# Optimization experiments

Measured on AMD Instinct MI355X. Metric: run time of the kernel, lower is better.

Reference implementation:

```python
import jax, jax.numpy as jnp
import numpy as np

N, F_IN, F_OUT, K = 4096, 32, 32, 2
NEG_SLOPE = 0.2
MASK_VAL = -9e15


def _sparse_mat(kv, km, density=0.01):
    vals = jax.random.normal(kv, (N, N), dtype=jnp.float32)
    mask = jax.random.uniform(km, (N, N)) < density
    return vals * mask


def setup_inputs() -> dict:
    key = jax.random.key(0)
    ks = jax.random.split(key, 12)
    x = jax.random.normal(ks[0], (N, F_IN), dtype=jnp.float32)
    Ld = _sparse_mat(ks[1], ks[2])
    Lu = _sparse_mat(ks[3], ks[4])
    P = jax.random.normal(ks[5], (N, N), dtype=jnp.float32) / np.sqrt(N)
    W1 = jax.random.normal(ks[6], (K, F_IN, F_OUT), dtype=jnp.float32) * 0.1
    W2 = jax.random.normal(ks[7], (K, F_IN, F_OUT), dtype=jnp.float32) * 0.1
    W0 = jax.random.normal(ks[8], (F_IN, F_OUT), dtype=jnp.float32) * 0.1
    att1 = jax.random.normal(ks[9], (2 * F_OUT * K, 1), dtype=jnp.float32) * 0.1
    att2 = jax.random.normal(ks[10], (2 * F_OUT * K, 1), dtype=jnp.float32) * 0.1
    return {"x": x, "Ld": Ld, "Lu": Lu, "P": P, "W1": W1, "W2": W2,
            "W0": W0, "att1": att1, "att2": att2}


def _branch(x, L, W, att):
    # W: [K, F_in, F_out]; precompute x @ W[k] for all k -> [K, N, F_out]
    Kk, _, Fo = W.shape
    xw = jnp.einsum('nf,kfo->kno', x, W)
    # torch.cat([x@W[k]], dim=1) == transpose+reshape of xw
    xcat = jnp.transpose(xw, (1, 0, 2)).reshape(x.shape[0], Kk * Fo)
    d = Fo * Kk
    e = xcat @ att[:d] + (xcat @ att[d:]).T            # [N, N]
    e = jax.nn.leaky_relu(e, negative_slope=NEG_SLOPE)
    e = jnp.where(L != 0, e, MASK_VAL)
    alpha = jax.nn.softmax(e, axis=1)                   # row softmax, no dropout (eval)
    z = alpha @ xw[0]
    a = alpha
    for k in range(1, Kk):
        a = a @ L
        z = z + a @ xw[k]
    return z


def reference(x, Ld, Lu, P, W1, W2, W0, att1, att2):
    z1 = _branch(x, Ld, W1, att1)
    z2 = _branch(x, Lu, W2, att2)
    x0 = P @ (x @ W0)
    return z1 + z2 + x0
```

## Files before the change

kernel.cpp:

```cpp
#include <hip/hip_runtime.h>
#include <hip/hip_bf16.h>

#define NN 4096
#define CAP 128
#define KS 8

typedef __attribute__((ext_vector_type(8))) short bf16x8;
typedef __attribute__((ext_vector_type(4))) float f32x4;

__device__ __forceinline__ float lrelu(float v) { return v >= 0.f ? v : 0.2f * v; }

__device__ __forceinline__ ushort f2bu(float f) {
    unsigned u = __float_as_uint(f);
    return (ushort)((u + 0x7FFFu + ((u >> 16) & 1u)) >> 16);
}

__global__ __launch_bounds__(256) void k_prep(
    const float* __restrict__ x,
    const float* __restrict__ W1, const float* __restrict__ W2,
    const float* __restrict__ W0,
    const float* __restrict__ att1, const float* __restrict__ att2,
    float* __restrict__ xwA1, float* __restrict__ xwB1,
    float* __restrict__ xwA2, float* __restrict__ xwB2,
    float* __restrict__ a1, float* __restrict__ b1,
    float* __restrict__ a2, float* __restrict__ b2,
    __hip_bfloat16* __restrict__ Bt)
{
    __shared__ float wl[5120];
    __shared__ float xs[256];
    const int t = threadIdx.x;
    for (int i = t; i < 2048; i += 256) { wl[i] = W1[i]; wl[2048 + i] = W2[i]; }
    for (int i = t; i < 1024; i += 256) wl[4096 + i] = W0[i];
    const int rowBase = blockIdx.x * 8;
    xs[t] = x[rowBase * 32 + t];
    __syncthreads();

    const int o = t & 31, r = t >> 5;
    const int row = rowBase + r;
    const float* xr = &xs[r * 32];
    float vA1 = 0.f, vB1 = 0.f, vA2 = 0.f, vB2 = 0.f, v0 = 0.f;
#pragma unroll
    for (int f = 0; f < 32; ++f) {
        const float xv = xr[f];
        vA1 += xv * wl[f * 32 + o];
        vB1 += xv * wl[1024 + f * 32 + o];
        vA2 += xv * wl[2048 + f * 32 + o];
        vB2 += xv * wl[3072 + f * 32 + o];
        v0  += xv * wl[4096 + f * 32 + o];
    }
    xwA1[row * 32 + o] = vA1;
    xwB1[row * 32 + o] = vB1;
    xwA2[row * 32 + o] = vA2;
    xwB2[row * 32 + o] = vB2;
    ((ushort*)Bt)[(size_t)o * NN + row] = f2bu(v0);

    float pa1 = vA1 * att1[o]      + vB1 * att1[32 + o];
    float pb1 = vA1 * att1[64 + o] + vB1 * att1[96 + o];
    float pa2 = vA2 * att2[o]      + vB2 * att2[32 + o];
    float pb2 = vA2 * att2[64 + o] + vB2 * att2[96 + o];
#pragma unroll
    for (int m = 1; m <= 16; m <<= 1) {
        pa1 += __shfl_xor(pa1, m); pb1 += __shfl_xor(pb1, m);
        pa2 += __shfl_xor(pa2, m); pb2 += __shfl_xor(pb2, m);
    }
    if (o == 0) { a1[row] = pa1; b1[row] = pb1; a2[row] = pa2; b2[row] = pb2; }
}

__global__ __launch_bounds__(256) void k_scan(
    const float* __restrict__ Ld, const float* __restrict__ Lu,
    const float* __restrict__ xwB1, const float* __restrict__ xwB2,
    int* __restrict__ csr, int* __restrict__ cntArr,
    float* __restrict__ y1, float* __restrict__ y2)
{
    const int row = blockIdx.x;
    const int br  = blockIdx.y;
    const float* L   = br ? Lu : Ld;
    const float* xwB = br ? xwB2 : xwB1;
    int*   csrB = csr + (size_t)br * NN * CAP;
    int*   cntB = cntArr + br * NN;
    float* y    = br ? y2 : y1;

    __shared__ int   sidx[CAP];
    __shared__ float sval[CAP];
    __shared__ int   scnt;
    __shared__ float red[256];
    const int t = threadIdx.x;
    const int lane = t & 63;
    if (t == 0) scnt = 0;
    __syncthreads();

    const float4* L4 = (const float4*)(L + (size_t)row * NN);
    float4 v[4];
#pragma unroll
    for (int it = 0; it < 4; ++it) v[it] = L4[it * 256 + t];

    const unsigned long long lt = (1ull << lane) - 1ull;
#pragma unroll
    for (int it = 0; it < 4; ++it) {
        const float vx = v[it].x, vy = v[it].y, vz = v[it].z, vw = v[it].w;
        const unsigned long long m0 = __ballot(vx != 0.f);
        const unsigned long long m1 = __ballot(vy != 0.f);
        const unsigned long long m2 = __ballot(vz != 0.f);
        const unsigned long long m3 = __ballot(vw != 0.f);
        const int p0 = __popcll(m0), p1 = __popcll(m1), p2 = __popcll(m2);
        const int tot = p0 + p1 + p2 + __popcll(m3);
        int base = 0;
        if (lane == 0 && tot) base = atomicAdd(&scnt, tot);
        base = __shfl(base, 0);
        const int c0 = (it * 256 + t) * 4;
        int s;
        s = base + __popcll(m0 & lt);
        if (vx != 0.f && s < CAP) { sidx[s] = c0;     sval[s] = vx; }
        s = base + p0 + __popcll(m1 & lt);
        if (vy != 0.f && s < CAP) { sidx[s] = c0 + 1; sval[s] = vy; }
        s = base + p0 + p1 + __popcll(m2 & lt);
        if (vz != 0.f && s < CAP) { sidx[s] = c0 + 2; sval[s] = vz; }
        s = base + p0 + p1 + p2 + __popcll(m3 & lt);
        if (vw != 0.f && s < CAP) { sidx[s] = c0 + 3; sval[s] = vw; }
    }
    __syncthreads();
    const int cnt = min(scnt, CAP);
    for (int s = t; s < cnt; s += 256) csrB[(size_t)row * CAP + s] = sidx[s];
    if (t == 0) cntB[row] = cnt;

    const int o = t & 31, g = t >> 5;
    float acc = 0.f;
    for (int s = g; s < cnt; s += 8) acc += sval[s] * xwB[(size_t)sidx[s] * 32 + o];
    red[t] = acc;
    __syncthreads();
    if (t < 32) {
        float tot2 = 0.f;
#pragma unroll
        for (int g2 = 0; g2 < 8; ++g2) tot2 += red[g2 * 32 + t];
        y[(size_t)row * 32 + t] = tot2;
    }
}

__global__ __launch_bounds__(256) void k_attn(
    const int* __restrict__ csr, const int* __restrict__ cntArr,
    const float* __restrict__ a1, const float* __restrict__ b1,
    const float* __restrict__ a2, const float* __restrict__ b2,
    const float* __restrict__ xwA1, const float* __restrict__ xwA2,
    const float* __restrict__ y1, const float* __restrict__ y2,
    float* __restrict__ z1, float* __restrict__ z2)
{
    const int br = blockIdx.y;
    const int* csrB = csr + (size_t)br * NN * CAP;
    const int* cntB = cntArr + br * NN;
    const float* aA  = br ? a2 : a1;
    const float* bA  = br ? b2 : b1;
    const float* xwA = br ? xwA2 : xwA1;
    const float* y   = br ? y2 : y1;
    float* z = br ? z2 : z1;

    __shared__ float elds[4 * CAP];
    const int w = threadIdx.x >> 6, lane = threadIdx.x & 63;
    const int row = blockIdx.x * 4 + w;
    const int cnt = cntB[row];
    const float ai = aA[row];
    const int* ci = csrB + (size_t)row * CAP;
    float* ew = elds + w * CAP;

    float lmax = -1e30f;
    for (int s = lane; s < cnt; s += 64) {
        const float e = lrelu(ai + bA[ci[s]]);
        ew[s] = e;
        lmax = fmaxf(lmax, e);
    }
#pragma unroll
    for (int m = 1; m <= 32; m <<= 1) lmax = fmaxf(lmax, __shfl_xor(lmax, m));
    float ssum = 0.f;
    for (int s = lane; s < cnt; s += 64) ssum += __expf(ew[s] - lmax);
#pragma unroll
    for (int m = 1; m <= 32; m <<= 1) ssum += __shfl_xor(ssum, m);

    const int h = lane >> 5, o = lane & 31;
    float acc = 0.f;
    for (int s = h; s < cnt; s += 2) {
        const float wgt = __expf(ew[s] - lmax);
        const int col = ci[s];
        acc += wgt * (xwA[(size_t)col * 32 + o] + y[(size_t)col * 32 + o]);
    }
    acc += __shfl_xor(acc, 32);
    if (lane < 32) z[(size_t)row * 32 + o] = (cnt > 0) ? acc / ssum : 0.f;
}

__global__ __launch_bounds__(256) void k_pgemm(
    const float* __restrict__ P, const ushort* __restrict__ Bt,
    float* __restrict__ partial)
{
    __shared__ ushort sA[2][16 * 64 * 8];
    __shared__ ushort sB[2][8 * 64 * 8];
    const int t = threadIdx.x;
    const int row0 = blockIdx.x * 64;
    const int ks = blockIdx.y;
    const float4*  P4  = (const float4*)P;
    const ushort4* Bt4 = (const ushort4*)Bt;

    const int lane = t & 63, w = t >> 6;

    f32x4 acc0 = {0.f, 0.f, 0.f, 0.f};
    f32x4 acc1 = {0.f, 0.f, 0.f, 0.f};

    auto stageA = [&](int c, int buf) {
        const int kc4 = (ks * 512 + c * 128) >> 2;
#pragma unroll
        for (int j = 0; j < 8; ++j) {
            const int i = t + 256 * j;
            const int row = i >> 5, q = i & 31;
            const float4 v = P4[(size_t)(row0 + row) * 1024 + kc4 + q];
            ushort4 u;
            u.x = f2bu(v.x); u.y = f2bu(v.y); u.z = f2bu(v.z); u.w = f2bu(v.w);
            const int wi = row >> 4, m = row & 15;
            const int kk = q >> 3, quad = (q >> 1) & 3, jj = q & 1;
            *(ushort4*)&sA[buf][(((wi * 4 + kk) * 64) + quad * 16 + m) * 8 + jj * 4] = u;
        }
    };
    auto stageB = [&](int c, int buf) {
        const int kc4 = (ks * 512 + c * 128) >> 2;
#pragma unroll
        for (int j = 0; j < 4; ++j) {
            const int i = t + 256 * j;
            const int o = i >> 5, q = i & 31;
            const ushort4 u = Bt4[(size_t)o * 1024 + kc4 + q];
            const int nt = o >> 4, n = o & 15;
            const int kk = q >> 3, quad = (q >> 1) & 3, jj = q & 1;
            *(ushort4*)&sB[buf][(((kk * 2 + nt) * 64) + quad * 16 + n) * 8 + jj * 4] = u;
        }
    };
    auto compute = [&](int buf) {
        const ushort* pa = &sA[buf][(w * 4) * 64 * 8 + lane * 8];
        const ushort* pb = &sB[buf][lane * 8];
#pragma unroll
        for (int kk = 0; kk < 4; ++kk) {
            const bf16x8 a  = *(const bf16x8*)(pa + kk * 512);
            const bf16x8 b0 = *(const bf16x8*)(pb + kk * 1024);
            const bf16x8 b1 = *(const bf16x8*)(pb + kk * 1024 + 512);
            acc0 = __builtin_amdgcn_mfma_f32_16x16x32_bf16(a, b0, acc0, 0, 0, 0);
            acc1 = __builtin_amdgcn_mfma_f32_16x16x32_bf16(a, b1, acc1, 0, 0, 0);
        }
    };

    stageA(0, 0); stageB(0, 0);
    __syncthreads();
    for (int c = 0; c < 4; ++c) {
        if (c < 3) { stageA(c + 1, (c + 1) & 1); stageB(c + 1, (c + 1) & 1); }
        compute(c & 1);
        __syncthreads();
    }

    const int m = lane & 15, quad = lane >> 4;
    float* out = partial + ((size_t)ks * NN + row0 + w * 16 + quad * 4) * 32;
#pragma unroll
    for (int r = 0; r < 4; ++r) {
        out[r * 32 + m]      = acc0[r];
        out[r * 32 + 16 + m] = acc1[r];
    }
}

__global__ __launch_bounds__(256) void k_combine(
    const float4* __restrict__ z1, const float4* __restrict__ z2,
    const float4* __restrict__ partial, float4* __restrict__ out)
{
    const int i = blockIdx.x * 256 + threadIdx.x;
    const float4 a = z1[i], b = z2[i];
    float rx = a.x + b.x, ry = a.y + b.y, rz = a.z + b.z, rw = a.w + b.w;
#pragma unroll
    for (int p = 0; p < KS; ++p) {
        const float4 c = partial[p * 32768 + i];
        rx += c.x; ry += c.y; rz += c.z; rw += c.w;
    }
    float4 rr; rr.x = rx; rr.y = ry; rr.z = rz; rr.w = rw;
    out[i] = rr;
}

extern "C" void kernel_launch(void* const* d_in, const int* in_sizes, int n_in,
                              void* d_out, int out_size, void* d_ws, size_t ws_size,
                              hipStream_t stream) {
    (void)in_sizes; (void)n_in; (void)out_size; (void)ws_size;
    const float* x    = (const float*)d_in[0];
    const float* Ld   = (const float*)d_in[1];
    const float* Lu   = (const float*)d_in[2];
    const float* P    = (const float*)d_in[3];
    const float* W1   = (const float*)d_in[4];
    const float* W2   = (const float*)d_in[5];
    const float* W0   = (const float*)d_in[6];
    const float* att1 = (const float*)d_in[7];
    const float* att2 = (const float*)d_in[8];

    float* ws = (float*)d_ws;
    float* xwA1 = ws;
    float* xwB1 = ws + 131072;
    float* xwA2 = ws + 262144;
    float* xwB2 = ws + 393216;
    float* y1   = ws + 524288;
    float* y2   = ws + 655360;
    float* z1   = ws + 786432;
    float* z2   = ws + 917504;
    float* a1   = ws + 1048576;
    float* b1   = ws + 1052672;
    float* a2   = ws + 1056768;
    float* b2   = ws + 1060864;
    float* partial = ws + 1064960;
    __hip_bfloat16* Bt = (__hip_bfloat16*)(ws + 1064960 + KS * 131072);
    int* csr = (int*)(ws + 1064960 + KS * 131072 + 65536);
    int* cnt = (int*)(ws + 1064960 + KS * 131072 + 65536 + 1048576);

    k_prep<<<512, 256, 0, stream>>>(x, W1, W2, W0, att1, att2,
                                    xwA1, xwB1, xwA2, xwB2, a1, b1, a2, b2, Bt);
    k_scan<<<dim3(NN, 2), 256, 0, stream>>>(Ld, Lu, xwB1, xwB2, csr, cnt, y1, y2);
    k_attn<<<dim3(NN / 4, 2), 256, 0, stream>>>(csr, cnt, a1, b1, a2, b2,
                                                xwA1, xwA2, y1, y2, z1, z2);
    k_pgemm<<<dim3(64, KS), 256, 0, stream>>>(P, (const ushort*)Bt, partial);
    k_combine<<<128, 256, 0, stream>>>((const float4*)z1, (const float4*)z2,
                                       (const float4*)partial, (float4*)d_out);
}
```

Before: 235.4 us.

## Make sparse scan deterministic, prefuse xwA into u, pipeline gathers

In k_scan, the LDS atomic slot allocation is replaced by a per-wave count prefix computed after one barrier, so compaction order becomes deterministic. Entries are zero-padded to a multiple of 16, and the gather-multiply loop is software-pipelined. The xwA term is added into the per-row y vector (now u), so k_attn gathers one array instead of two. k_attn also computes the softmax weights in registers with a fixed two-slot layout and prefetches its gathers a step ahead. The cost is redundant ballots in k_scan and extra work on padded zero entries.

```diff
diff --git a/kernel.cpp b/kernel.cpp
--- a/kernel.cpp
+++ b/kernel.cpp
@@ -69,25 +69,25 @@
 __global__ __launch_bounds__(256) void k_scan(
     const float* __restrict__ Ld, const float* __restrict__ Lu,
     const float* __restrict__ xwB1, const float* __restrict__ xwB2,
+    const float* __restrict__ xwA1, const float* __restrict__ xwA2,
     int* __restrict__ csr, int* __restrict__ cntArr,
-    float* __restrict__ y1, float* __restrict__ y2)
+    float* __restrict__ u1, float* __restrict__ u2)
 {
     const int row = blockIdx.x;
     const int br  = blockIdx.y;
     const float* L   = br ? Lu : Ld;
     const float* xwB = br ? xwB2 : xwB1;
+    const float* xwA = br ? xwA2 : xwA1;
     int*   csrB = csr + (size_t)br * NN * CAP;
     int*   cntB = cntArr + br * NN;
-    float* y    = br ? y2 : y1;
+    float* u    = br ? u2 : u1;
 
     __shared__ int   sidx[CAP];
     __shared__ float sval[CAP];
-    __shared__ int   scnt;
+    __shared__ int   wcnt[16];
     __shared__ float red[256];
     const int t = threadIdx.x;
-    const int lane = t & 63;
-    if (t == 0) scnt = 0;
-    __syncthreads();
+    const int lane = t & 63, w = t >> 6;
 
     const float4* L4 = (const float4*)(L + (size_t)row * NN);
     float4 v[4];
@@ -95,6 +95,38 @@
     for (int it = 0; it < 4; ++it) v[it] = L4[it * 256 + t];
 
     const unsigned long long lt = (1ull << lane) - 1ull;
+
+    int tots[4];
+#pragma unroll
+    for (int it = 0; it < 4; ++it) {
+        const unsigned long long m0 = __ballot(v[it].x != 0.f);
+        const unsigned long long m1 = __ballot(v[it].y != 0.f);
+        const unsigned long long m2 = __ballot(v[it].z != 0.f);
+        const unsigned long long m3 = __ballot(v[it].w != 0.f);
+        tots[it] = __popcll(m0) + __popcll(m1) + __popcll(m2) + __popcll(m3);
+    }
+    if (lane == 0) {
+        int4 tv; tv.x = tots[0]; tv.y = tots[1]; tv.z = tots[2]; tv.w = tots[3];
+        *(int4*)&wcnt[w * 4] = tv;
+    }
+    __syncthreads();
+
+    const int4 ca = *(const int4*)&wcnt[0];
+    const int4 cb = *(const int4*)&wcnt[4];
+    const int4 cc = *(const int4*)&wcnt[8];
+    const int4 cd = *(const int4*)&wcnt[12];
+    const int cs[16] = {ca.x, ca.y, ca.z, ca.w, cb.x, cb.y, cb.z, cb.w,
+                        cc.x, cc.y, cc.z, cc.w, cd.x, cd.y, cd.z, cd.w};
+    int total = 0;
+#pragma unroll
+    for (int k2 = 0; k2 < 16; ++k2) total += cs[k2];
+    int base = 0;
+#pragma unroll
+    for (int k2 = 0; k2 < 16; ++k2) base += (k2 < (w << 2)) ? cs[k2] : 0;
+
+    const int cnt  = min(total, CAP);
+    const int cp16 = min((cnt + 15) & ~15, CAP);
+
 #pragma unroll
     for (int it = 0; it < 4; ++it) {
         const float vx = v[it].x, vy = v[it].y, vz = v[it].z, vw = v[it].w;
@@ -103,10 +135,6 @@
         const unsigned long long m2 = __ballot(vz != 0.f);
         const unsigned long long m3 = __ballot(vw != 0.f);
         const int p0 = __popcll(m0), p1 = __popcll(m1), p2 = __popcll(m2);
-        const int tot = p0 + p1 + p2 + __popcll(m3);
-        int base = 0;
-        if (lane == 0 && tot) base = atomicAdd(&scnt, tot);
-        base = __shfl(base, 0);
         const int c0 = (it * 256 + t) * 4;
         int s;
         s = base + __popcll(m0 & lt);
@@ -117,22 +145,40 @@
         if (vz != 0.f && s < CAP) { sidx[s] = c0 + 2; sval[s] = vz; }
         s = base + p0 + p1 + p2 + __popcll(m3 & lt);
         if (vw != 0.f && s < CAP) { sidx[s] = c0 + 3; sval[s] = vw; }
-    }
-    __syncthreads();
-    const int cnt = min(scnt, CAP);
-    for (int s = t; s < cnt; s += 256) csrB[(size_t)row * CAP + s] = sidx[s];
-    if (t == 0) cntB[row] = cnt;
+        base += p0 + p1 + p2 + __popcll(m3);
+    }
+    if (t >= cnt && t < cp16) { sidx[t] = 0; sval[t] = 0.f; }
+    __syncthreads();
+
+    if (t < cp16) csrB[(size_t)row * CAP + t] = sidx[t];
+    if (t == 0)   cntB[row] = cnt;
 
     const int o = t & 31, g = t >> 5;
     float acc = 0.f;
-    for (int s = g; s < cnt; s += 8) acc += sval[s] * xwB[(size_t)sidx[s] * 32 + o];
+    const int nPair = cp16 >> 4;
+    if (nPair > 0) {
+        int   iA0 = sidx[g],      iA1 = sidx[g + 8];
+        float vA0 = sval[g],      vA1 = sval[g + 8];
+        float xA0 = xwB[(size_t)iA0 * 32 + o];
+        float xA1 = xwB[(size_t)iA1 * 32 + o];
+        for (int j = 1; j < nPair; ++j) {
+            const int sB = g + 16 * j;
+            const int   iB0 = sidx[sB],  iB1 = sidx[sB + 8];
+            const float vB0 = sval[sB],  vB1 = sval[sB + 8];
+            const float xB0 = xwB[(size_t)iB0 * 32 + o];
+            const float xB1 = xwB[(size_t)iB1 * 32 + o];
+            acc += vA0 * xA0 + vA1 * xA1;
+            vA0 = vB0; xA0 = xB0; vA1 = vB1; xA1 = xB1;
+        }
+        acc += vA0 * xA0 + vA1 * xA1;
+    }
     red[t] = acc;
     __syncthreads();
     if (t < 32) {
         float tot2 = 0.f;
 #pragma unroll
         for (int g2 = 0; g2 < 8; ++g2) tot2 += red[g2 * 32 + t];
-        y[(size_t)row * 32 + t] = tot2;
+        u[(size_t)row * 32 + t] = tot2 + xwA[(size_t)row * 32 + t];
     }
 }
 
@@ -140,46 +186,69 @@
     const int* __restrict__ csr, const int* __restrict__ cntArr,
     const float* __restrict__ a1, const float* __restrict__ b1,
     const float* __restrict__ a2, const float* __restrict__ b2,
-    const float* __restrict__ xwA1, const float* __restrict__ xwA2,
-    const float* __restrict__ y1, const float* __restrict__ y2,
+    const float* __restrict__ u1, const float* __restrict__ u2,
     float* __restrict__ z1, float* __restrict__ z2)
 {
     const int br = blockIdx.y;
     const int* csrB = csr + (size_t)br * NN * CAP;
     const int* cntB = cntArr + br * NN;
-    const float* aA  = br ? a2 : a1;
-    const float* bA  = br ? b2 : b1;
-    const float* xwA = br ? xwA2 : xwA1;
-    const float* y   = br ? y2 : y1;
+    const float* aA = br ? a2 : a1;
+    const float* bA = br ? b2 : b1;
+    const float* U  = br ? u2 : u1;
     float* z = br ? z2 : z1;
 
-    __shared__ float elds[4 * CAP];
+    __shared__ float sw[4 * CAP];
+    __shared__ int   sci[4 * CAP];
     const int w = threadIdx.x >> 6, lane = threadIdx.x & 63;
     const int row = blockIdx.x * 4 + w;
     const int cnt = cntB[row];
+    const int cp16 = min((cnt + 15) & ~15, CAP);
     const float ai = aA[row];
     const int* ci = csrB + (size_t)row * CAP;
-    float* ew = elds + w * CAP;
-
-    float lmax = -1e30f;
-    for (int s = lane; s < cnt; s += 64) {
-        const float e = lrelu(ai + bA[ci[s]]);
-        ew[s] = e;
-        lmax = fmaxf(lmax, e);
-    }
+    float* swg = sw + w * CAP;
+    int*   scg = sci + w * CAP;
+
+    int id0 = 0, id1 = 0;
+    if (lane < cp16)      id0 = ci[lane];
+    if (lane + 64 < cp16) id1 = ci[lane + 64];
+    float e0 = (lane < cnt)      ? lrelu(ai + bA[id0]) : -1e30f;
+    float e1 = (lane + 64 < cnt) ? lrelu(ai + bA[id1]) : -1e30f;
+    float lmax = fmaxf(e0, e1);
 #pragma unroll
     for (int m = 1; m <= 32; m <<= 1) lmax = fmaxf(lmax, __shfl_xor(lmax, m));
-    float ssum = 0.f;
-    for (int s = lane; s < cnt; s += 64) ssum += __expf(ew[s] - lmax);
+    const float w0 = __expf(e0 - lmax), w1 = __expf(e1 - lmax);
+    float ssum = w0 + w1;
 #pragma unroll
     for (int m = 1; m <= 32; m <<= 1) ssum += __shfl_xor(ssum, m);
-
-    const int h = lane >> 5, o = lane & 31;
+    swg[lane] = w0; swg[lane + 64] = w1;
+    scg[lane] = id0; scg[lane + 64] = id1;
+
+    const int o = lane & 31, h = lane >> 5;
     float acc = 0.f;
-    for (int s = h; s < cnt; s += 2) {
-        const float wgt = __expf(ew[s] - lmax);
-        const int col = ci[s];
-        acc += wgt * (xwA[(size_t)col * 32 + o] + y[(size_t)col * 32 + o]);
+    const int nb = cp16 >> 3;
+    if (cnt > 0) {
+        float wgA[4], uvA[4];
+#pragma unroll
+        for (int q = 0; q < 4; ++q) {
+            const int s = h + 2 * q;
+            wgA[q] = swg[s];
+            uvA[q] = U[(size_t)scg[s] * 32 + o];
+        }
+        for (int j = 1; j < nb; ++j) {
+            float wgB[4], uvB[4];
+#pragma unroll
+            for (int q = 0; q < 4; ++q) {
+                const int s = h + 8 * j + 2 * q;
+                wgB[q] = swg[s];
+                uvB[q] = U[(size_t)scg[s] * 32 + o];
+            }
+#pragma unroll
+            for (int q = 0; q < 4; ++q) acc += wgA[q] * uvA[q];
+#pragma unroll
+            for (int q = 0; q < 4; ++q) { wgA[q] = wgB[q]; uvA[q] = uvB[q]; }
+        }
+#pragma unroll
+        for (int q = 0; q < 4; ++q) acc += wgA[q] * uvA[q];
     }
     acc += __shfl_xor(acc, 32);
     if (lane < 32) z[(size_t)row * 32 + o] = (cnt > 0) ? acc / ssum : 0.f;
@@ -293,8 +362,8 @@
     float* xwB1 = ws + 131072;
     float* xwA2 = ws + 262144;
     float* xwB2 = ws + 393216;
-    float* y1   = ws + 524288;
-    float* y2   = ws + 655360;
+    float* u1   = ws + 524288;
+    float* u2   = ws + 655360;
     float* z1   = ws + 786432;
     float* z2   = ws + 917504;
     float* a1   = ws + 1048576;
@@ -308,9 +377,10 @@
 
     k_prep<<<512, 256, 0, stream>>>(x, W1, W2, W0, att1, att2,
                                     xwA1, xwB1, xwA2, xwB2, a1, b1, a2, b2, Bt);
-    k_scan<<<dim3(NN, 2), 256, 0, stream>>>(Ld, Lu, xwB1, xwB2, csr, cnt, y1, y2);
+    k_scan<<<dim3(NN, 2), 256, 0, stream>>>(Ld, Lu, xwB1, xwB2, xwA1, xwA2,
+                                            csr, cnt, u1, u2);
     k_attn<<<dim3(NN / 4, 2), 256, 0, stream>>>(csr, cnt, a1, b1, a2, b2,
-                                                xwA1, xwA2, y1, y2, z1, z2);
+                                                u1, u2, z1, z2);
     k_pgemm<<<dim3(64, KS), 256, 0, stream>>>(P, (const ushort*)Bt, partial);
     k_combine<<<128, 256, 0, stream>>>((const float4*)z1, (const float4*)z2,
                                        (const float4*)partial, (float4*)d_out);
```

Measured after the change: 225.8 us. 4.1% less time.
